# Kernel optimization log

Measured on AMD Instinct MI355X. Metric: run time of the kernel, lower is better.

The kernel has to match this reference:

```python
import jax, jax.numpy as jnp
import numpy as np

N_ATOMS = 200000   # total atoms across batch of molecules
N_BONDS = 400000   # total directed bonds
HSIZE   = 256      # mpn_size
MLP     = 512      # mlp_size
BS_OUT  = 5        # bond edit classes (bs_outdim)
N_MOLS  = 1000     # batch of molecules (len(atom_scope))


def _p(k, shape, scale):
    return jax.random.normal(k, shape, jnp.float32) * scale


def setup_inputs() -> dict:
    key = jax.random.key(0)
    ks = jax.random.split(key, 12)
    s_h = 1.0 / np.sqrt(HSIZE).astype(np.float32)
    s_2h = 1.0 / np.sqrt(2 * HSIZE).astype(np.float32)
    s_m = 1.0 / np.sqrt(MLP).astype(np.float32)
    return {
        'c_atom':  jax.random.normal(ks[0], (N_ATOMS, HSIZE), jnp.float32),
        'ha_prev': jax.random.normal(ks[1], (N_ATOMS, HSIZE), jnp.float32),
        'W_vv':    jnp.eye(HSIZE, dtype=jnp.float32),  # nn.init.eye_ in original
        'W_vc':    _p(ks[2], (HSIZE, HSIZE), s_h),
        'bond_W1': _p(ks[3], (2 * HSIZE, MLP), s_2h),
        'bond_b1': jnp.zeros((MLP,), jnp.float32),
        'bond_W2': _p(ks[4], (MLP, BS_OUT), s_m),
        'bond_b2': jnp.zeros((BS_OUT,), jnp.float32),
        'uni_W1':  _p(ks[5], (HSIZE, MLP), s_h),
        'uni_b1':  jnp.zeros((MLP,), jnp.float32),
        'uni_W2':  _p(ks[6], (MLP, 1), s_m),
        'uni_b2':  jnp.zeros((1,), jnp.float32),
        'done_W1': _p(ks[7], (HSIZE, MLP), s_h),
        'done_b1': jnp.zeros((MLP,), jnp.float32),
        'done_W2': _p(ks[8], (MLP, 1), s_m),
        'done_b2': jnp.zeros((1,), jnp.float32),
        'mol_id':     jax.random.randint(ks[9], (N_ATOMS,), 0, N_MOLS, jnp.int32),
        'bond_index': jax.random.randint(ks[10], (N_BONDS, 2), 0, N_ATOMS, jnp.int32),
    }


def _mlp(x, W1, b1, W2, b2):
    # build_mlp: Linear -> ReLU -> (dropout, off at eval) -> Linear
    return jax.nn.relu(x @ W1 + b1) @ W2 + b2


def reference(c_atom, ha_prev, W_vv, W_vc,
              bond_W1, bond_b1, bond_W2, bond_b2,
              uni_W1, uni_b1, uni_W2, uni_b2,
              done_W1, done_b1, done_W2, done_b2,
              mol_id, bond_index):
    # ha = relu(W_vv @ ha_prev + W_vc @ c_atom); ha[0] = 0 (padding atom)
    ha = jax.nn.relu(ha_prev @ W_vv + c_atom @ W_vc)
    ha = ha.at[0].set(0.0)
    # per-molecule pooling (replaces python loop over atom_scope)
    hm = jax.ops.segment_sum(ha, mol_id, num_segments=N_MOLS)  # [N_MOLS, H]
    # gather bond endpoint embeddings (index_select_ND)
    bond_in = jnp.concatenate([ha[bond_index[:, 0]], ha[bond_index[:, 1]]], axis=-1)  # [E, 2H]
    bond_logits = _mlp(bond_in, bond_W1, bond_b1, bond_W2, bond_b2)  # [E, BS_OUT]
    uni_logits = _mlp(ha, uni_W1, uni_b1, uni_W2, uni_b2)            # [N, 1]
    done_logits = _mlp(hm, done_W1, done_b1, done_W2, done_b2)       # [M, 1]
    # edit_logits in original is a ragged per-mol concat of these three;
    # return the dense flat concatenation (same values, fixed shape)
    return jnp.concatenate([bond_logits.ravel(), uni_logits.ravel(), done_logits.ravel()])
```

## Files before the change

### kernel.cpp

```cpp
#include <hip/hip_runtime.h>
#include <hip/hip_bf16.h>

typedef __attribute__((ext_vector_type(8))) short bf16x8;
typedef __attribute__((ext_vector_type(4))) float f32x4;

static __device__ __forceinline__ unsigned short f2bf(float f) {
    union { float f; unsigned u; } v; v.f = f;
    unsigned r = v.u + 0x7fffu + ((v.u >> 16) & 1u);
    return (unsigned short)(r >> 16);
}

#define GLOAD16(g, l) __builtin_amdgcn_global_load_lds( \
    (const __attribute__((address_space(1))) void*)(g), \
    (__attribute__((address_space(3))) void*)(l), 16, 0, 0)

__global__ __launch_bounds__(256) void conv_weights(
    const float* __restrict__ Wvv, const float* __restrict__ Wvc,
    const float* __restrict__ bW1, const float* __restrict__ uW1,
    unsigned short* __restrict__ WcT, unsigned short* __restrict__ bW1T,
    unsigned short* __restrict__ uW1T)
{
    int idx = blockIdx.x * 256 + threadIdx.x;
    if (idx < 131072) {
        int n = idx & 255, k = idx >> 8;
        float s = (k < 256) ? Wvv[k * 256 + n] : Wvc[(k - 256) * 256 + n];
        WcT[((k >> 3) * 256 + n) * 8 + (k & 7)] = f2bf(s);
    } else if (idx < 131072 + 262144) {
        int t = idx - 131072;
        int n = t & 511, k = t >> 9;
        bW1T[((k >> 3) * 512 + n) * 8 + (k & 7)] = f2bf(bW1[k * 512 + n]);
    } else if (idx < 131072 + 262144 + 131072) {
        int t = idx - 393216;
        int n = t & 511, k = t >> 9;
        uW1T[((k >> 3) * 512 + n) * 8 + (k & 7)] = f2bf(uW1[k * 512 + n]);
    }
}

__global__ __launch_bounds__(512, 4) void ha_kernel(
    const float* __restrict__ ha_prev, const float* __restrict__ c_atom,
    const unsigned short* __restrict__ WcT, const int* __restrict__ mol_id,
    unsigned short* __restrict__ haB, float* __restrict__ hm, int NA)
{
    __shared__ __align__(16) unsigned short As[2][128 * 64];

    const int tid = threadIdx.x;
    const int wv = tid >> 6, lane = tid & 63;
    const int wr = wv >> 2, wc = wv & 3;
    const int c15 = lane & 15, kq = lane >> 4;
    const int xm3 = (c15 & 7) << 3;
    const int m0 = blockIdx.x * 128;

    const int cr0 = tid >> 3, chc = tid & 7;
    const int cr1 = (512 + tid) >> 3;
    int row0 = m0 + cr0; if (row0 >= NA) row0 = NA - 1;
    int row1 = m0 + cr1; if (row1 >= NA) row1 = NA - 1;

    f32x4 v00, v01, v10, v11;
    #define HA_LOAD(ks) { \
        const float* src = ((ks) < 4) ? ha_prev : c_atom; \
        const int kb = ((ks) & 3) * 64 + chc * 8; \
        const float* s0 = src + (size_t)row0 * 256 + kb; \
        const float* s1 = src + (size_t)row1 * 256 + kb; \
        v00 = *(const f32x4*)s0; v01 = *(const f32x4*)(s0 + 4); \
        v10 = *(const f32x4*)s1; v11 = *(const f32x4*)(s1 + 4); }
    #define HA_WRITE(buf) { \
        bf16x8 p0, p1; \
        p0[0]=(short)f2bf(v00[0]); p0[1]=(short)f2bf(v00[1]); p0[2]=(short)f2bf(v00[2]); p0[3]=(short)f2bf(v00[3]); \
        p0[4]=(short)f2bf(v01[0]); p0[5]=(short)f2bf(v01[1]); p0[6]=(short)f2bf(v01[2]); p0[7]=(short)f2bf(v01[3]); \
        p1[0]=(short)f2bf(v10[0]); p1[1]=(short)f2bf(v10[1]); p1[2]=(short)f2bf(v10[2]); p1[3]=(short)f2bf(v10[3]); \
        p1[4]=(short)f2bf(v11[0]); p1[5]=(short)f2bf(v11[1]); p1[6]=(short)f2bf(v11[2]); p1[7]=(short)f2bf(v11[3]); \
        *(bf16x8*)&As[buf][cr0 * 64 + ((chc * 8) ^ ((cr0 & 7) << 3))] = p0; \
        *(bf16x8*)&As[buf][cr1 * 64 + ((chc * 8) ^ ((cr1 & 7) << 3))] = p1; }

    f32x4 acc[4][4];
#pragma unroll
    for (int m = 0; m < 4; ++m)
#pragma unroll
        for (int n = 0; n < 4; ++n) acc[m][n] = (f32x4){0.f, 0.f, 0.f, 0.f};

    HA_LOAD(0); HA_WRITE(0);
    __syncthreads();

    for (int ks = 0; ks < 8; ++ks) {
        if (ks < 7) HA_LOAD(ks + 1);
        const int buf = ks & 1;
#pragma unroll
        for (int kk = 0; kk < 2; ++kk) {
            bf16x8 aF[4], bF[4];
            const int plane = ks * 8 + kk * 4 + kq;
#pragma unroll
            for (int n = 0; n < 4; ++n)
                bF[n] = *(const bf16x8*)(WcT + ((size_t)plane * 256 + wc * 64 + n * 16 + c15) * 8);
#pragma unroll
            for (int m = 0; m < 4; ++m)
                aF[m] = *(const bf16x8*)&As[buf][(wr * 64 + m * 16 + c15) * 64 + ((kk * 32 + kq * 8) ^ xm3)];
#pragma unroll
            for (int m = 0; m < 4; ++m)
#pragma unroll
                for (int n = 0; n < 4; ++n)
                    acc[m][n] = __builtin_amdgcn_mfma_f32_16x16x32_bf16(aF[m], bF[n], acc[m][n], 0, 0, 0);
        }
        if (ks < 7) HA_WRITE((ks + 1) & 1);
        __syncthreads();
    }

#pragma unroll
    for (int m = 0; m < 4; ++m) {
#pragma unroll
        for (int reg = 0; reg < 4; ++reg) {
            int row = m0 + wr * 64 + m * 16 + kq * 4 + reg;
            if (row >= NA) continue;
            bool z = (row == 0);
            int mol = z ? 0 : mol_id[row];
#pragma unroll
            for (int n = 0; n < 4; ++n) {
                int col = wc * 64 + n * 16 + c15;
                float v = fmaxf(acc[m][n][reg], 0.f);
                if (z) v = 0.f;
                haB[(size_t)row * 256 + col] = f2bf(v);
                if (!z) atomicAdd(&hm[mol * 256 + col], v);
            }
        }
    }
}

__global__ __launch_bounds__(512, 4) void bond_kernel(
    const unsigned short* __restrict__ haB, const int* __restrict__ bidx,
    const unsigned short* __restrict__ bW1T, const float* __restrict__ b1,
    const float* __restrict__ W2, const float* __restrict__ b2,
    float* __restrict__ outB, int NB)
{
    __shared__ __align__(16) unsigned short As[8 * 64 * 64];
    __shared__ float obuf[64][5];

    const int tid = threadIdx.x;
    const int wv = tid >> 6, lane = tid & 63;
    const int c15 = lane & 15, kq = lane >> 4;
    const int b0 = blockIdx.x * 64;

    if (tid < 320) ((float*)obuf)[tid] = 0.f;

    {
        const int ep = wv >> 2, koff = (wv & 3) * 64;
        const int rsub = lane >> 3, csub = lane & 7;
        int eidxs[8];
#pragma unroll
        for (int j = 0; j < 8; ++j) {
            int gb = b0 + j * 8 + rsub; if (gb >= NB) gb = 0;
            eidxs[j] = bidx[gb * 2 + ep];
        }
#pragma unroll
        for (int j = 0; j < 8; ++j) {
            int r = j * 8 + rsub;
            GLOAD16(haB + (size_t)eidxs[j] * 256 + koff + (size_t)((csub ^ (r & 7)) * 8),
                    As + wv * 4096 + j * 512);
        }
    }
    __syncthreads();

    f32x4 acc[4][4];
#pragma unroll
    for (int m = 0; m < 4; ++m)
#pragma unroll
        for (int n = 0; n < 4; ++n) acc[m][n] = (f32x4){0.f, 0.f, 0.f, 0.f};

    bf16x8 breg[2][4];
    {
        const int pl0 = kq;
#pragma unroll
        for (int n = 0; n < 4; ++n)
            breg[0][n] = *(const bf16x8*)(bW1T + ((size_t)pl0 * 512 + wv * 64 + n * 16 + c15) * 8);
    }
#pragma unroll
    for (int s = 0; s < 16; ++s) {
        if (s < 15) {
            const int pl = ((s + 1) >> 1) * 8 + ((s + 1) & 1) * 4 + kq;
#pragma unroll
            for (int n = 0; n < 4; ++n)
                breg[(s + 1) & 1][n] = *(const bf16x8*)(bW1T + ((size_t)pl * 512 + wv * 64 + n * 16 + c15) * 8);
        }
        const int ks = s >> 1, kk = s & 1;
        bf16x8 aF[4];
#pragma unroll
        for (int m = 0; m < 4; ++m) {
            int r = m * 16 + c15;
            aF[m] = *(const bf16x8*)&As[ks * 4096 + r * 64 + (((kk * 4 + kq) ^ (r & 7)) * 8)];
        }
#pragma unroll
        for (int m = 0; m < 4; ++m)
#pragma unroll
            for (int n = 0; n < 4; ++n)
                acc[m][n] = __builtin_amdgcn_mfma_f32_16x16x32_bf16(aF[m], breg[s & 1][n], acc[m][n], 0, 0, 0);
    }

    float b1c[4], w2c[4][5];
#pragma unroll
    for (int n = 0; n < 4; ++n) {
        int col = wv * 64 + n * 16 + c15;
        b1c[n] = b1[col];
#pragma unroll
        for (int j = 0; j < 5; ++j) w2c[n][j] = W2[col * 5 + j];
    }
#pragma unroll
    for (int m = 0; m < 4; ++m) {
#pragma unroll
        for (int reg = 0; reg < 4; ++reg) {
            float s[5] = {0.f, 0.f, 0.f, 0.f, 0.f};
#pragma unroll
            for (int n = 0; n < 4; ++n) {
                float p = fmaxf(acc[m][n][reg] + b1c[n], 0.f);
#pragma unroll
                for (int j = 0; j < 5; ++j) s[j] += p * w2c[n][j];
            }
#pragma unroll
            for (int off = 1; off < 16; off <<= 1)
#pragma unroll
                for (int j = 0; j < 5; ++j) s[j] += __shfl_xor(s[j], off);
            if (c15 == 0) {
                int rl = m * 16 + kq * 4 + reg;
#pragma unroll
                for (int j = 0; j < 5; ++j) atomicAdd(&obuf[rl][j], s[j]);
            }
        }
    }
    __syncthreads();
    {
        int r = tid >> 3, j = tid & 7;
        if (j < 5) {
            int row = b0 + r;
            if (row < NB) outB[(size_t)row * 5 + j] = obuf[r][j] + b2[j];
        }
    }
}

__global__ __launch_bounds__(512, 4) void uni_kernel(
    const unsigned short* __restrict__ haB, const unsigned short* __restrict__ uW1T,
    const float* __restrict__ b1, const float* __restrict__ W2,
    const float* __restrict__ b2, float* __restrict__ outU, int NA)
{
    __shared__ __align__(16) unsigned short As[4 * 64 * 64];
    __shared__ float obuf[64];

    const int tid = threadIdx.x;
    const int wv = tid >> 6, lane = tid & 63;
    const int c15 = lane & 15, kq = lane >> 4;
    const int a0 = blockIdx.x * 64;

    if (tid < 64) obuf[tid] = 0.f;

    {
        const int kt = wv >> 1, koff = kt * 64;
        const int rsub = lane >> 3, csub = lane & 7;
#pragma unroll
        for (int jj = 0; jj < 4; ++jj) {
            int j = (wv & 1) * 4 + jj;
            int r = j * 8 + rsub;
            int ga = a0 + r; if (ga >= NA) ga = NA - 1;
            GLOAD16(haB + (size_t)ga * 256 + koff + (size_t)((csub ^ (r & 7)) * 8),
                    As + kt * 4096 + j * 512);
        }
    }
    __syncthreads();

    f32x4 acc[4][4];
#pragma unroll
    for (int m = 0; m < 4; ++m)
#pragma unroll
        for (int n = 0; n < 4; ++n) acc[m][n] = (f32x4){0.f, 0.f, 0.f, 0.f};

    bf16x8 breg[2][4];
    {
        const int pl0 = kq;
#pragma unroll
        for (int n = 0; n < 4; ++n)
            breg[0][n] = *(const bf16x8*)(uW1T + ((size_t)pl0 * 512 + wv * 64 + n * 16 + c15) * 8);
    }
#pragma unroll
    for (int s = 0; s < 8; ++s) {
        if (s < 7) {
            const int pl = ((s + 1) >> 1) * 8 + ((s + 1) & 1) * 4 + kq;
#pragma unroll
            for (int n = 0; n < 4; ++n)
                breg[(s + 1) & 1][n] = *(const bf16x8*)(uW1T + ((size_t)pl * 512 + wv * 64 + n * 16 + c15) * 8);
        }
        const int ks = s >> 1, kk = s & 1;
        bf16x8 aF[4];
#pragma unroll
        for (int m = 0; m < 4; ++m) {
            int r = m * 16 + c15;
            aF[m] = *(const bf16x8*)&As[ks * 4096 + r * 64 + (((kk * 4 + kq) ^ (r & 7)) * 8)];
        }
#pragma unroll
        for (int m = 0; m < 4; ++m)
#pragma unroll
            for (int n = 0; n < 4; ++n)
                acc[m][n] = __builtin_amdgcn_mfma_f32_16x16x32_bf16(aF[m], breg[s & 1][n], acc[m][n], 0, 0, 0);
    }

    float b1c[4], w2c[4];
#pragma unroll
    for (int n = 0; n < 4; ++n) {
        int col = wv * 64 + n * 16 + c15;
        b1c[n] = b1[col];
        w2c[n] = W2[col];
    }
#pragma unroll
    for (int m = 0; m < 4; ++m) {
#pragma unroll
        for (int reg = 0; reg < 4; ++reg) {
            float s = 0.f;
#pragma unroll
            for (int n = 0; n < 4; ++n)
                s += fmaxf(acc[m][n][reg] + b1c[n], 0.f) * w2c[n];
#pragma unroll
            for (int off = 1; off < 16; off <<= 1) s += __shfl_xor(s, off);
            if (c15 == 0) atomicAdd(&obuf[m * 16 + kq * 4 + reg], s);
        }
    }
    __syncthreads();
    if (tid < 64) {
        int row = a0 + tid;
        if (row < NA) outU[row] = obuf[tid] + b2[0];
    }
}

__global__ __launch_bounds__(256) void done_kernel(
    const float* __restrict__ hm, const float* __restrict__ W1,
    const float* __restrict__ b1, const float* __restrict__ W2,
    const float* __restrict__ b2, float* __restrict__ outD, int NM)
{
    __shared__ float rsh[4][256];
    __shared__ float red[4][4];
    const int tid = threadIdx.x;
    const int wv = tid >> 6, lane = tid & 63;
    const int mol0 = blockIdx.x * 4;
#pragma unroll
    for (int q = 0; q < 4; ++q)
        rsh[q][tid] = (mol0 + q < NM) ? hm[(size_t)(mol0 + q) * 256 + tid] : 0.f;
    __syncthreads();
    float h[4][2];
#pragma unroll
    for (int q = 0; q < 4; ++q) { h[q][0] = 0.f; h[q][1] = 0.f; }
    for (int k = 0; k < 256; ++k) {
        float w0 = W1[k * 512 + tid];
        float w1 = W1[k * 512 + tid + 256];
#pragma unroll
        for (int q = 0; q < 4; ++q) {
            h[q][0] += rsh[q][k] * w0;
            h[q][1] += rsh[q][k] * w1;
        }
    }
    float bb0 = b1[tid], bb1v = b1[tid + 256];
    float ww0 = W2[tid], ww1 = W2[tid + 256];
#pragma unroll
    for (int q = 0; q < 4; ++q) {
        float p = fmaxf(h[q][0] + bb0, 0.f) * ww0 + fmaxf(h[q][1] + bb1v, 0.f) * ww1;
#pragma unroll
        for (int off = 1; off < 64; off <<= 1) p += __shfl_xor(p, off);
        if (lane == 0) red[q][wv] = p;
    }
    __syncthreads();
    if (tid < 4 && mol0 + tid < NM)
        outD[mol0 + tid] = red[tid][0] + red[tid][1] + red[tid][2] + red[tid][3] + b2[0];
}

extern "C" void kernel_launch(void* const* d_in, const int* in_sizes, int n_in,
                              void* d_out, int out_size, void* d_ws, size_t ws_size,
                              hipStream_t stream)
{
    const float* c_atom  = (const float*)d_in[0];
    const float* ha_prev = (const float*)d_in[1];
    const float* W_vv    = (const float*)d_in[2];
    const float* W_vc    = (const float*)d_in[3];
    const float* bW1     = (const float*)d_in[4];
    const float* bb1     = (const float*)d_in[5];
    const float* bW2     = (const float*)d_in[6];
    const float* bb2     = (const float*)d_in[7];
    const float* uW1     = (const float*)d_in[8];
    const float* ub1     = (const float*)d_in[9];
    const float* uW2     = (const float*)d_in[10];
    const float* ub2     = (const float*)d_in[11];
    const float* dW1     = (const float*)d_in[12];
    const float* db1     = (const float*)d_in[13];
    const float* dW2     = (const float*)d_in[14];
    const float* db2     = (const float*)d_in[15];
    const int* mol_id    = (const int*)d_in[16];
    const int* bidx      = (const int*)d_in[17];

    const int H = 256, BS = 5;
    const int NA = in_sizes[0] / H;
    const int NB = in_sizes[17] / 2;
    const int NM = out_size - NB * BS - NA;

    float* out  = (float*)d_out;
    float* outB = out;
    float* outU = out + (size_t)NB * BS;
    float* outD = outU + NA;

    char* ws = (char*)d_ws;
    size_t off = 0;
    unsigned short* haB = (unsigned short*)(ws + off);
    off += (size_t)NA * H * 2;            off = (off + 255) & ~(size_t)255;
    float* hm = (float*)(ws + off);
    off += (size_t)NM * H * 4;            off = (off + 255) & ~(size_t)255;
    unsigned short* WcT = (unsigned short*)(ws + off);
    off += (size_t)131072 * 2;            off = (off + 255) & ~(size_t)255;
    unsigned short* bW1T = (unsigned short*)(ws + off);
    off += (size_t)262144 * 2;            off = (off + 255) & ~(size_t)255;
    unsigned short* uW1T = (unsigned short*)(ws + off);

    hipMemsetAsync(hm, 0, (size_t)NM * H * 4, stream);
    conv_weights<<<2048, 256, 0, stream>>>(W_vv, W_vc, bW1, uW1, WcT, bW1T, uW1T);
    ha_kernel<<<(NA + 127) / 128, 512, 0, stream>>>(ha_prev, c_atom, WcT, mol_id, haB, hm, NA);
    bond_kernel<<<(NB + 63) / 64, 512, 0, stream>>>(haB, bidx, bW1T, bb1, bW2, bb2, outB, NB);
    uni_kernel<<<(NA + 63) / 64, 512, 0, stream>>>(haB, uW1T, ub1, uW2, ub2, outU, NA);
    done_kernel<<<(NM + 3) / 4, 256, 0, stream>>>(hm, dW1, db1, dW2, db2, outD, NM);
}
```

Before: 650.9 us.

## Precompute per-atom first-layer projections in FP8 and stream bond MLP

The first bond MLP layer is split algebraically: [ha_i, ha_j]·W1 = ha_i·W1a + ha_j·W1b. A per-atom GEMM over 200k atoms computes these projections once instead of a GEMM over 400k gathered bonds. The projections are stored as FP8 to cut memory traffic. A wave-per-bond streaming kernel then gathers the two projected rows, adds them, applies ReLU and the second layer. The uni MLP gets the same treatment, and the code falls back to the GEMM path when the workspace is too small. FP8 storage of pre-activation values adds quantization error that may exceed tolerance.

```diff
diff --git a/kernel.cpp b/kernel.cpp
--- a/kernel.cpp
+++ b/kernel.cpp
@@ -1,5 +1,6 @@
 #include <hip/hip_runtime.h>
 #include <hip/hip_bf16.h>
+#include <math.h>
 
 typedef __attribute__((ext_vector_type(8))) short bf16x8;
 typedef __attribute__((ext_vector_type(4))) float f32x4;
@@ -14,25 +15,74 @@
     (const __attribute__((address_space(1))) void*)(g), \
     (__attribute__((address_space(3))) void*)(l), 16, 0, 0)
 
+#if defined(__has_builtin)
+#  if __has_builtin(__builtin_amdgcn_cvt_pk_fp8_f32) && __has_builtin(__builtin_amdgcn_cvt_pk_f32_fp8)
+#    define HAVE_FP8_CVT 1
+#  endif
+#endif
+#ifndef HAVE_FP8_CVT
+#  define HAVE_FP8_CVT 0
+#endif
+
+static __device__ __forceinline__ float f8dec_sw(unsigned b) {
+    unsigned s = b >> 7, e = (b >> 3) & 15, m = b & 7;
+    float v = e ? ldexpf((float)(8 + m), (int)e - 10) : ldexpf((float)m, -9);
+    return s ? -v : v;
+}
+static __device__ __forceinline__ unsigned char f8enc_sw(float x) {
+    union { float f; unsigned u; } v; v.f = x;
+    unsigned s = (v.u >> 31) << 7;
+    float ax = fabsf(x);
+    if (ax >= 448.f) return (unsigned char)(s | 0x7E);
+    if (ax < 0.015625f) { int m = (int)(ax * 512.f + 0.5f); return (unsigned char)(s | m); }
+    int e; float fr = frexpf(ax, &e);
+    int q = (int)(fr * 16.f + 0.5f);
+    if (q == 16) { q = 8; e += 1; }
+    if (e - 1 > 8) return (unsigned char)(s | 0x7E);
+    return (unsigned char)(s | ((e - 1 + 7) << 3) | (q - 8));
+}
+static __device__ __forceinline__ unsigned char f8e(float v) {
+#if HAVE_FP8_CVT
+    return (unsigned char)(__builtin_amdgcn_cvt_pk_fp8_f32(v, v, 0, false) & 0xFF);
+#else
+    return f8enc_sw(v);
+#endif
+}
+static __device__ __forceinline__ void f8d2_lo(unsigned w, float& x, float& y) {
+#if HAVE_FP8_CVT
+    auto r = __builtin_amdgcn_cvt_pk_f32_fp8((int)w, false);
+    x = r[0]; y = r[1];
+#else
+    x = f8dec_sw(w & 0xFF); y = f8dec_sw((w >> 8) & 0xFF);
+#endif
+}
+static __device__ __forceinline__ void f8d2_hi(unsigned w, float& x, float& y) {
+#if HAVE_FP8_CVT
+    auto r = __builtin_amdgcn_cvt_pk_f32_fp8((int)w, true);
+    x = r[0]; y = r[1];
+#else
+    x = f8dec_sw((w >> 16) & 0xFF); y = f8dec_sw((w >> 24) & 0xFF);
+#endif
+}
+
 __global__ __launch_bounds__(256) void conv_weights(
     const float* __restrict__ Wvv, const float* __restrict__ Wvc,
     const float* __restrict__ bW1, const float* __restrict__ uW1,
-    unsigned short* __restrict__ WcT, unsigned short* __restrict__ bW1T,
-    unsigned short* __restrict__ uW1T)
+    unsigned short* __restrict__ WcT, unsigned short* __restrict__ WgT)
 {
     int idx = blockIdx.x * 256 + threadIdx.x;
     if (idx < 131072) {
         int n = idx & 255, k = idx >> 8;
         float s = (k < 256) ? Wvv[k * 256 + n] : Wvc[(k - 256) * 256 + n];
         WcT[((k >> 3) * 256 + n) * 8 + (k & 7)] = f2bf(s);
-    } else if (idx < 131072 + 262144) {
+    } else {
         int t = idx - 131072;
-        int n = t & 511, k = t >> 9;
-        bW1T[((k >> 3) * 512 + n) * 8 + (k & 7)] = f2bf(bW1[k * 512 + n]);
-    } else if (idx < 131072 + 262144 + 131072) {
-        int t = idx - 393216;
-        int n = t & 511, k = t >> 9;
-        uW1T[((k >> 3) * 512 + n) * 8 + (k & 7)] = f2bf(uW1[k * 512 + n]);
+        int k = t / 1536, n2 = t - k * 1536;
+        float s;
+        if (n2 < 512)       s = bW1[k * 512 + n2];
+        else if (n2 < 1024) s = bW1[(256 + k) * 512 + (n2 - 512)];
+        else                s = uW1[k * 512 + (n2 - 1024)];
+        WgT[((k >> 3) * 1536 + n2) * 8 + (k & 7)] = f2bf(s);
     }
 }
 
@@ -124,9 +174,190 @@
     }
 }
 
-__global__ __launch_bounds__(512, 4) void bond_kernel(
+__global__ __launch_bounds__(1024, 4) void g_kernel(
+    const unsigned short* __restrict__ haB, const unsigned short* __restrict__ WgT,
+    unsigned char* __restrict__ G, unsigned char* __restrict__ Hu, int NA)
+{
+    __shared__ __align__(16) unsigned short As[4][128][64];
+
+    const int tid = threadIdx.x;
+    const int wv = tid >> 6, lane = tid & 63;
+    const int wr = wv >> 3, wc = wv & 7;
+    const int c15 = lane & 15, kq = lane >> 4;
+    const int a0 = blockIdx.x * 128;
+    const int nb = blockIdx.y;
+
+    {
+        const int kt = wv >> 2;
+        const int rsub = lane >> 3, csub = lane & 7;
+#pragma unroll
+        for (int j = 0; j < 4; ++j) {
+            int rg = (wv & 3) * 4 + j;
+            int r = rg * 8 + rsub;
+            int ga = a0 + r; if (ga >= NA) ga = NA - 1;
+            GLOAD16(haB + (size_t)ga * 256 + kt * 64 + (size_t)((csub ^ (r & 7)) * 8),
+                    &As[kt][rg * 8][0]);
+        }
+    }
+    __syncthreads();
+
+    f32x4 acc[4][4];
+#pragma unroll
+    for (int m = 0; m < 4; ++m)
+#pragma unroll
+        for (int n = 0; n < 4; ++n) acc[m][n] = (f32x4){0.f, 0.f, 0.f, 0.f};
+
+    bf16x8 breg[2][4];
+#pragma unroll
+    for (int n = 0; n < 4; ++n)
+        breg[0][n] = *(const bf16x8*)(WgT + ((size_t)kq * 1536 + nb * 512 + wc * 64 + n * 16 + c15) * 8);
+
+#pragma unroll
+    for (int s = 0; s < 8; ++s) {
+        if (s < 7) {
+            const int pl = (s + 1) * 4 + kq;
+#pragma unroll
+            for (int n = 0; n < 4; ++n)
+                breg[(s + 1) & 1][n] = *(const bf16x8*)(WgT + ((size_t)pl * 1536 + nb * 512 + wc * 64 + n * 16 + c15) * 8);
+        }
+        const int ks = s >> 1, kk = s & 1;
+        bf16x8 aF[4];
+#pragma unroll
+        for (int m = 0; m < 4; ++m) {
+            int r = wr * 64 + m * 16 + c15;
+            aF[m] = *(const bf16x8*)&As[ks][r][((kk * 4 + kq) ^ (r & 7)) * 8];
+        }
+#pragma unroll
+        for (int m = 0; m < 4; ++m)
+#pragma unroll
+            for (int n = 0; n < 4; ++n)
+                acc[m][n] = __builtin_amdgcn_mfma_f32_16x16x32_bf16(aF[m], breg[s & 1][n], acc[m][n], 0, 0, 0);
+    }
+
+    unsigned char* dst; int rstride;
+    if (nb < 2) { dst = G + nb * 512; rstride = 1024; }
+    else        { dst = Hu;           rstride = 512;  }
+#pragma unroll
+    for (int m = 0; m < 4; ++m) {
+#pragma unroll
+        for (int reg = 0; reg < 4; ++reg) {
+            int row = a0 + wr * 64 + m * 16 + kq * 4 + reg;
+            if (row >= NA) continue;
+#pragma unroll
+            for (int n = 0; n < 4; ++n) {
+                int col = wc * 64 + n * 16 + c15;
+                dst[(size_t)row * rstride + col] = f8e(acc[m][n][reg]);
+            }
+        }
+    }
+}
+
+__global__ __launch_bounds__(256) void bond_stream(
+    const unsigned char* __restrict__ G, const int* __restrict__ bidx,
+    const float* __restrict__ b1, const float* __restrict__ W2,
+    const float* __restrict__ b2, float* __restrict__ outB, int NB, int nwaves)
+{
+    const int lane = threadIdx.x & 63;
+    const int wid = (blockIdx.x * blockDim.x + threadIdx.x) >> 6;
+
+    float b1c[8], w2c[8][5];
+#pragma unroll
+    for (int i = 0; i < 8; ++i) {
+        int h = lane * 8 + i;
+        b1c[i] = b1[h];
+#pragma unroll
+        for (int j = 0; j < 5; ++j) w2c[i][j] = W2[h * 5 + j];
+    }
+    float bb[5];
+#pragma unroll
+    for (int j = 0; j < 5; ++j) bb[j] = b2[j];
+
+    int e = wid;
+    if (e >= NB) return;
+    int2 ep = ((const int2*)bidx)[e];
+    int2 epN = (e + nwaves < NB) ? ((const int2*)bidx)[e + nwaves] : ep;
+    uint2 ga = *(const uint2*)(G + (size_t)ep.x * 1024 + lane * 8);
+    uint2 gb = *(const uint2*)(G + (size_t)ep.y * 1024 + 512 + lane * 8);
+
+    while (e < NB) {
+        int en = e + nwaves;
+        uint2 gaN, gbN; int2 epN2 = epN;
+        if (en < NB) {
+            gaN = *(const uint2*)(G + (size_t)epN.x * 1024 + lane * 8);
+            gbN = *(const uint2*)(G + (size_t)epN.y * 1024 + 512 + lane * 8);
+            int e2 = en + nwaves;
+            if (e2 < NB) epN2 = ((const int2*)bidx)[e2];
+        }
+        float s[5] = {0.f, 0.f, 0.f, 0.f, 0.f};
+#pragma unroll
+        for (int half = 0; half < 2; ++half) {
+            unsigned wa = half ? ga.y : ga.x;
+            unsigned wb = half ? gb.y : gb.x;
+            float a0v, a1v, a2v, a3v, b0v, b1v, b2v, b3v;
+            f8d2_lo(wa, a0v, a1v); f8d2_hi(wa, a2v, a3v);
+            f8d2_lo(wb, b0v, b1v); f8d2_hi(wb, b2v, b3v);
+            float hv[4] = { a0v + b0v, a1v + b1v, a2v + b2v, a3v + b3v };
+#pragma unroll
+            for (int t = 0; t < 4; ++t) {
+                int i = half * 4 + t;
+                float p = fmaxf(hv[t] + b1c[i], 0.f);
+#pragma unroll
+                for (int j = 0; j < 5; ++j) s[j] += p * w2c[i][j];
+            }
+        }
+#pragma unroll
+        for (int off = 1; off < 64; off <<= 1)
+#pragma unroll
+            for (int j = 0; j < 5; ++j) s[j] += __shfl_xor(s[j], off);
+        if (lane == 0) {
+#pragma unroll
+            for (int j = 0; j < 5; ++j) outB[(size_t)e * 5 + j] = s[j] + bb[j];
+        }
+        e = en; ga = gaN; gb = gbN; epN = epN2;
+    }
+}
+
+__global__ __launch_bounds__(256) void uni_stream(
+    const unsigned char* __restrict__ Hu, const float* __restrict__ b1,
+    const float* __restrict__ W2, const float* __restrict__ b2,
+    float* __restrict__ outU, int NA, int nwaves)
+{
+    const int lane = threadIdx.x & 63;
+    const int wid = (blockIdx.x * blockDim.x + threadIdx.x) >> 6;
+
+    float b1c[8], w2c[8];
+#pragma unroll
+    for (int i = 0; i < 8; ++i) {
+        int h = lane * 8 + i;
+        b1c[i] = b1[h];
+        w2c[i] = W2[h];
+    }
+    float bb = b2[0];
+
+    for (int a = wid; a < NA; a += nwaves) {
+        uint2 g = *(const uint2*)(Hu + (size_t)a * 512 + lane * 8);
+        float s = 0.f;
+#pragma unroll
+        for (int half = 0; half < 2; ++half) {
+            unsigned w = half ? g.y : g.x;
+            float v0, v1, v2, v3;
+            f8d2_lo(w, v0, v1); f8d2_hi(w, v2, v3);
+            float hv[4] = { v0, v1, v2, v3 };
+#pragma unroll
+            for (int t = 0; t < 4; ++t) {
+                int i = half * 4 + t;
+                s += fmaxf(hv[t] + b1c[i], 0.f) * w2c[i];
+            }
+        }
+#pragma unroll
+        for (int off = 1; off < 64; off <<= 1) s += __shfl_xor(s, off);
+        if (lane == 0) outU[a] = s + bb;
+    }
+}
+
+__global__ __launch_bounds__(512, 4) void bond_gemm(
     const unsigned short* __restrict__ haB, const int* __restrict__ bidx,
-    const unsigned short* __restrict__ bW1T, const float* __restrict__ b1,
+    const unsigned short* __restrict__ WgT, const float* __restrict__ b1,
     const float* __restrict__ W2, const float* __restrict__ b2,
     float* __restrict__ outB, int NB)
 {
@@ -146,8 +377,8 @@
         int eidxs[8];
 #pragma unroll
         for (int j = 0; j < 8; ++j) {
-            int gb = b0 + j * 8 + rsub; if (gb >= NB) gb = 0;
-            eidxs[j] = bidx[gb * 2 + ep];
+            int gbd = b0 + j * 8 + rsub; if (gbd >= NB) gbd = 0;
+            eidxs[j] = bidx[gbd * 2 + ep];
         }
 #pragma unroll
         for (int j = 0; j < 8; ++j) {
@@ -165,19 +396,16 @@
         for (int n = 0; n < 4; ++n) acc[m][n] = (f32x4){0.f, 0.f, 0.f, 0.f};
 
     bf16x8 breg[2][4];
-    {
-        const int pl0 = kq;
-#pragma unroll
-        for (int n = 0; n < 4; ++n)
-            breg[0][n] = *(const bf16x8*)(bW1T + ((size_t)pl0 * 512 + wv * 64 + n * 16 + c15) * 8);
-    }
+#pragma unroll
+    for (int n = 0; n < 4; ++n)
+        breg[0][n] = *(const bf16x8*)(WgT + ((size_t)(kq & 31) * 1536 + (kq >> 5) * 512 + wv * 64 + n * 16 + c15) * 8);
 #pragma unroll
     for (int s = 0; s < 16; ++s) {
         if (s < 15) {
-            const int pl = ((s + 1) >> 1) * 8 + ((s + 1) & 1) * 4 + kq;
-#pragma unroll
-            for (int n = 0; n < 4; ++n)
-                breg[(s + 1) & 1][n] = *(const bf16x8*)(bW1T + ((size_t)pl * 512 + wv * 64 + n * 16 + c15) * 8);
+            const int pl = (s + 1) * 4 + kq;
+#pragma unroll
+            for (int n = 0; n < 4; ++n)
+                breg[(s + 1) & 1][n] = *(const bf16x8*)(WgT + ((size_t)(pl & 31) * 1536 + (pl >> 5) * 512 + wv * 64 + n * 16 + c15) * 8);
         }
         const int ks = s >> 1, kk = s & 1;
         bf16x8 aF[4];
@@ -234,7 +462,7 @@
 }
 
 __global__ __launch_bounds__(512, 4) void uni_kernel(
-    const unsigned short* __restrict__ haB, const unsigned short* __restrict__ uW1T,
+    const unsigned short* __restrict__ haB, const unsigned short* __restrict__ WgT,
     const float* __restrict__ b1, const float* __restrict__ W2,
     const float* __restrict__ b2, float* __restrict__ outU, int NA)
 {
@@ -269,19 +497,16 @@
         for (int n = 0; n < 4; ++n) acc[m][n] = (f32x4){0.f, 0.f, 0.f, 0.f};
 
     bf16x8 breg[2][4];
-    {
-        const int pl0 = kq;
-#pragma unroll
-        for (int n = 0; n < 4; ++n)
-            breg[0][n] = *(const bf16x8*)(uW1T + ((size_t)pl0 * 512 + wv * 64 + n * 16 + c15) * 8);
-    }
+#pragma unroll
+    for (int n = 0; n < 4; ++n)
+        breg[0][n] = *(const bf16x8*)(WgT + ((size_t)kq * 1536 + 1024 + wv * 64 + n * 16 + c15) * 8);
 #pragma unroll
     for (int s = 0; s < 8; ++s) {
         if (s < 7) {
-            const int pl = ((s + 1) >> 1) * 8 + ((s + 1) & 1) * 4 + kq;
-#pragma unroll
-            for (int n = 0; n < 4; ++n)
-                breg[(s + 1) & 1][n] = *(const bf16x8*)(uW1T + ((size_t)pl * 512 + wv * 64 + n * 16 + c15) * 8);
+            const int pl = (s + 1) * 4 + kq;
+#pragma unroll
+            for (int n = 0; n < 4; ++n)
+                breg[(s + 1) & 1][n] = *(const bf16x8*)(WgT + ((size_t)pl * 1536 + 1024 + wv * 64 + n * 16 + c15) * 8);
         }
         const int ks = s >> 1, kk = s & 1;
         bf16x8 aF[4];
@@ -405,14 +630,31 @@
     off += (size_t)NM * H * 4;            off = (off + 255) & ~(size_t)255;
     unsigned short* WcT = (unsigned short*)(ws + off);
     off += (size_t)131072 * 2;            off = (off + 255) & ~(size_t)255;
-    unsigned short* bW1T = (unsigned short*)(ws + off);
-    off += (size_t)262144 * 2;            off = (off + 255) & ~(size_t)255;
-    unsigned short* uW1T = (unsigned short*)(ws + off);
+    unsigned short* WgT = (unsigned short*)(ws + off);
+    off += (size_t)393216 * 2;            off = (off + 255) & ~(size_t)255;
+    unsigned char* G = (unsigned char*)(ws + off);
+    size_t need_G = off + (size_t)NA * 1024;
+    size_t offHu = (need_G + 255) & ~(size_t)255;
+    unsigned char* Hu = (unsigned char*)(ws + offHu);
+    size_t need_Hu = offHu + (size_t)NA * 512;
+
+    const bool hasG  = ws_size >= need_G;
+    const bool hasHu = ws_size >= need_Hu;
 
     hipMemsetAsync(hm, 0, (size_t)NM * H * 4, stream);
-    conv_weights<<<2048, 256, 0, stream>>>(W_vv, W_vc, bW1, uW1, WcT, bW1T, uW1T);
+    conv_weights<<<2048, 256, 0, stream>>>(W_vv, W_vc, bW1, uW1, WcT, WgT);
     ha_kernel<<<(NA + 127) / 128, 512, 0, stream>>>(ha_prev, c_atom, WcT, mol_id, haB, hm, NA);
-    bond_kernel<<<(NB + 63) / 64, 512, 0, stream>>>(haB, bidx, bW1T, bb1, bW2, bb2, outB, NB);
-    uni_kernel<<<(NA + 63) / 64, 512, 0, stream>>>(haB, uW1T, ub1, uW2, ub2, outU, NA);
+
+    if (hasG) {
+        g_kernel<<<dim3((NA + 127) / 128, hasHu ? 3 : 2), 1024, 0, stream>>>(haB, WgT, G, Hu, NA);
+        bond_stream<<<2048, 256, 0, stream>>>(G, bidx, bb1, bW2, bb2, outB, NB, 2048 * 4);
+        if (hasHu)
+            uni_stream<<<1024, 256, 0, stream>>>(Hu, ub1, uW2, ub2, outU, NA, 1024 * 4);
+        else
+            uni_kernel<<<(NA + 63) / 64, 512, 0, stream>>>(haB, WgT, ub1, uW2, ub2, outU, NA);
+    } else {
+        bond_gemm<<<(NB + 63) / 64, 512, 0, stream>>>(haB, bidx, WgT, bb1, bW2, bb2, outB, NB);
+        uni_kernel<<<(NA + 63) / 64, 512, 0, stream>>>(haB, WgT, ub1, uW2, ub2, outU, NA);
+    }
     done_kernel<<<(NM + 3) / 4, 256, 0, stream>>>(hm, dW1, db1, dW2, db2, outD, NM);
 }
```

Result: slower. 697.5 us (+7.2%).
